# Kernel tuning notes

Measured on AMD Instinct MI355X. Metric: run time of the kernel, lower is better.

The kernel has to match this reference:

```python
import jax, jax.numpy as jnp
import numpy as np

B, N, S, T, H = 4, 6000, 48, 550, 128  # events, electrons, sensor grid, ticks, mlp hidden
INV_2PI = 1.0 / (2.0 * 3.14159)  # matches the source constant 3.14159
GAUSS_NORM = 0.3989422804


def setup_inputs() -> dict:
    key = jax.random.key(0)
    ks = jax.random.split(key, 9)
    simulator_input = jax.random.normal(ks[0], (B, N, 2), dtype=jnp.float32)
    z_positions = jax.random.uniform(ks[1], (B, N), dtype=jnp.float32) * (T - 1)
    mask = jnp.ones((B, N, 1), dtype=jnp.float32)
    # 48x48 sensor plane spanning [-5, 5] in x and y
    lin = jnp.linspace(-5.0, 5.0, S, dtype=jnp.float32)
    sensor_locations = jnp.stack(jnp.meshgrid(lin, lin, indexing='ij'), axis=-1)  # [S,S,2]
    # MLP params (2 -> H -> H -> 1)
    W1 = jax.random.normal(ks[2], (2, H), dtype=jnp.float32) * (1.0 / np.sqrt(2.0))
    b1 = jnp.zeros((H,), dtype=jnp.float32)
    W2 = jax.random.normal(ks[3], (H, H), dtype=jnp.float32) * (1.0 / np.sqrt(H))
    b2 = jnp.zeros((H,), dtype=jnp.float32)
    W3 = jax.random.normal(ks[4], (H, 1), dtype=jnp.float32) * (1.0 / np.sqrt(H))
    b3 = jnp.zeros((1,), dtype=jnp.float32)
    el_spread = jnp.ones((1,), dtype=jnp.float32)
    nn_bin_sigma = jnp.ones((1,), dtype=jnp.float32)
    return {
        'simulator_input': simulator_input, 'z_positions': z_positions, 'mask': mask,
        'sensor_locations': sensor_locations,
        'W1': W1, 'b1': b1, 'W2': W2, 'b2': b2, 'W3': W3, 'b3': b3,
        'el_spread': el_spread, 'nn_bin_sigma': nn_bin_sigma,
    }


def reference(simulator_input, z_positions, mask, sensor_locations,
              W1, b1, W2, b2, W3, b3, el_spread, nn_bin_sigma):
    # EL simulator MLP -> exp -> mask  ([B,N,1])
    h = jax.nn.relu(simulator_input @ W1 + b1)
    h = jax.nn.relu(h @ W2 + b2)
    resp = jnp.exp(h @ W3 + b3) * mask

    # Spatial gaussian splat onto sensor plane: [B,N,S,S]
    diff = simulator_input[:, :, None, None, :] - sensor_locations  # [B,N,S,S,2]
    r2 = jnp.sum(diff * diff, axis=-1)
    variance = el_spread ** 2  # (1,)
    spread = jnp.exp(-0.5 * (r2 / variance)) * (INV_2PI / variance)
    sr = spread * resp[..., None]  # [B,N,S,S]

    # Temporal gaussian over waveform ticks: [B,N,T]
    ticks = jnp.arange(T, dtype=simulator_input.dtype)  # linspace(0, T-1, T)
    bs = nn_bin_sigma ** 2  # (1,)
    ev = jnp.exp(-((ticks[None, None, :] - z_positions[:, :, None]) ** 2) / (2.0 * bs))
    ev = ev * (GAUSS_NORM / jnp.sqrt(bs))

    # Matmul reduce over electrons, then sum over batch: [S,S,T]
    return jnp.einsum('bnpq,bnt->pqt', sr, ev)
```

## Files before the change

### kernel.cpp

```cpp
#include <hip/hip_runtime.h>
#include <math.h>

#define BB 4
#define NN 6000
#define BN (BB*NN)
#define SS 48
#define PQ (SS*SS)
#define TT 550
#define HH 128

#define TPQ 128
#define TTILE 64
#define NTILES 9
#define KT 16
#define SPLITK 8
#define CAP 6144
#define MLP_E 64

__device__ __constant__ float kINV_2PI = 1.0f / (2.0f * 3.14159f);
__device__ __constant__ float kGAUSS_NORM = 0.3989422804f;
#define LOG2E 1.4426950408889634f

__device__ __forceinline__ float fexp2(float x) { return __builtin_amdgcn_exp2f(x); }

__global__ __launch_bounds__(256) void prep_kernel(
    const float* __restrict__ si, const float* __restrict__ zpos,
    const float* __restrict__ mask,
    const float* __restrict__ W1, const float* __restrict__ b1,
    const float* __restrict__ W2, const float* __restrict__ b2,
    const float* __restrict__ W3, const float* __restrict__ b3,
    const float* __restrict__ sensor, const float* __restrict__ el_spread,
    const float* __restrict__ nn_bin_sigma,
    int* __restrict__ counts,
    float* __restrict__ GxT, float* __restrict__ GyT, float* __restrict__ zT)
{
  __shared__ float sh1T[HH][MLP_E];
  __shared__ float sW1[2 * HH];
  __shared__ float sb1[HH], sb2[HH], sW3[HH];
  __shared__ float sex[MLP_E], sey[MLP_E], sresp[MLP_E], slin[SS];
  __shared__ int   sSlot[NTILES][MLP_E];
  int tid = threadIdx.x;
  if (tid < 2 * HH) sW1[tid] = W1[tid];
  if (tid < HH) { sb1[tid] = b1[tid]; sb2[tid] = b2[tid]; sW3[tid] = W3[tid]; }
  if (tid < SS) slin[tid] = sensor[tid * SS * 2];
  int e0 = blockIdx.x * MLP_E;
  int e = tid & 63;
  float x0 = si[2 * (e0 + e)], x1 = si[2 * (e0 + e) + 1];
  if (tid < MLP_E) { sex[tid] = x0; sey[tid] = x1; }
  __syncthreads();
  int jb = (tid >> 6) * 32;
  #pragma unroll
  for (int jj = 0; jj < 32; ++jj) {
    int j = jb + jj;
    sh1T[j][e] = fmaxf(x0 * sW1[j] + x1 * sW1[HH + j] + sb1[j], 0.0f);
  }
  __syncthreads();
  int c4 = (tid & 31) * 4;
  int eh = tid >> 5;
  float acc[8][4] = {};
  for (int i = 0; i < HH; ++i) {
    float4 w  = *(const float4*)&W2[i * HH + c4];
    float4 ha = *(const float4*)&sh1T[i][eh * 8];
    float4 hb = *(const float4*)&sh1T[i][eh * 8 + 4];
    float hv[8] = {ha.x, ha.y, ha.z, ha.w, hb.x, hb.y, hb.z, hb.w};
    #pragma unroll
    for (int ee = 0; ee < 8; ++ee) {
      acc[ee][0] += hv[ee] * w.x; acc[ee][1] += hv[ee] * w.y;
      acc[ee][2] += hv[ee] * w.z; acc[ee][3] += hv[ee] * w.w;
    }
  }
  float outp[8];
  #pragma unroll
  for (int ee = 0; ee < 8; ++ee) {
    float sacc = 0.0f;
    #pragma unroll
    for (int cc = 0; cc < 4; ++cc)
      sacc += fmaxf(acc[ee][cc] + sb2[c4 + cc], 0.0f) * sW3[c4 + cc];
    outp[ee] = sacc;
  }
  #pragma unroll
  for (int off = 1; off < 32; off <<= 1)
    #pragma unroll
    for (int ee = 0; ee < 8; ++ee)
      outp[ee] += __shfl_xor(outp[ee], off);
  if ((tid & 31) == 0) {
    float b3v = b3[0];
    #pragma unroll
    for (int ee = 0; ee < 8; ++ee) {
      int eidx = e0 + eh * 8 + ee;
      sresp[eh * 8 + ee] = fexp2((outp[ee] + b3v) * LOG2E) * mask[eidx];
    }
  }
  __syncthreads();
  if (tid < 64) {
    float sbv = nn_bin_sigma[0];
    float bs = sbv * sbv;
    float Wz = ceilf(sqrtf(128.0f * bs));
    float z = zpos[e0 + tid];
    int jlo = (int)floorf((z - Wz) * (1.0f / TTILE));
    int jhi = (int)floorf((z + Wz) * (1.0f / TTILE));
    jlo = jlo < 0 ? 0 : jlo;
    jhi = jhi > NTILES - 1 ? NTILES - 1 : jhi;
    int lane = tid;
    for (int j = 0; j < NTILES; ++j) {
      bool c = (j >= jlo) && (j <= jhi);
      unsigned long long m = __ballot(c);
      int s = -1;
      if (m != 0ull) {
        int leader = __ffsll(m) - 1;
        int base = 0;
        if (lane == leader) base = atomicAdd(&counts[j], __popcll(m));
        base = __shfl(base, leader);
        if (c) {
          int slot = base + __popcll(m & ((1ull << lane) - 1ull));
          if (slot < CAP) { s = slot; zT[j * CAP + slot] = z; }
        }
      }
      sSlot[j][lane] = s;
    }
  }
  __syncthreads();
  float es = el_spread[0];
  float var = es * es;
  float c = (0.5f / var) * LOG2E;
  float sbv = nn_bin_sigma[0];
  float bs = sbv * sbv;
  float amul = (kINV_2PI / var) * (kGAUSS_NORM / sqrtf(bs));
  for (int v = tid; v < MLP_E * SS; v += 256) {
    int ei = v / SS;
    int p = v - ei * SS;
    float lp = slin[p];
    float dx = sex[ei] - lp, dy = sey[ei] - lp;
    float gx = fexp2(-dx * dx * c) * sresp[ei] * amul;
    float gy = fexp2(-dy * dy * c);
    #pragma unroll
    for (int j = 0; j < NTILES; ++j) {
      int s = sSlot[j][ei];
      if (s >= 0) {
        GxT[(j * CAP + s) * SS + p] = gx;
        GyT[(j * CAP + s) * SS + p] = gy;
      }
    }
  }
}

__global__ __launch_bounds__(256) void gemm_kernel(
    const float* __restrict__ GxT, const float* __restrict__ GyT,
    const float* __restrict__ zT, const int* __restrict__ counts,
    const float* __restrict__ nn_bin_sigma, float* __restrict__ part)
{
  __shared__ __attribute__((aligned(16))) float Asm[KT][TPQ];
  __shared__ __attribute__((aligned(16))) float Esm[KT][TTILE];

  int tid = threadIdx.x;
  int pqBase = blockIdx.x * TPQ;
  int tileT = blockIdx.y;
  int tBase = tileT * TTILE;
  int bz = blockIdx.z;

  float s = nn_bin_sigma[0];
  float c2 = (0.5f * LOG2E) / (s * s);

  int count = counts[tileT];
  if (count > CAP) count = CAP;
  int chunks = (count + KT - 1) / KT;
  int cpsBase = chunks / SPLITK;
  int rem = chunks - cpsBase * SPLITK;
  int myC = cpsBase + (bz < rem ? 1 : 0);
  int chunk0 = bz * cpsBase + (bz < rem ? bz : rem);
  int k0 = chunk0 * KT;
  int kend = k0 + myC * KT;

  const float* __restrict__ Gxb = GxT + tileT * CAP * SS;
  const float* __restrict__ Gyb = GyT + tileT * CAP * SS;
  const float* __restrict__ zb  = zT + tileT * CAP;

  int aR = tid >> 5;
  int aC = (tid & 31) * 4;
  int eR = tid >> 4;
  int eC = (tid & 15) * 4;
  int tpq = (tid >> 4) * 8;
  int tt  = (tid & 15) * 4;

  int pqc = pqBase + aC;
  int p0 = pqc / SS,       q0 = pqc - p0 * SS;
  int p1 = (pqc+1) / SS,   q1 = (pqc+1) - p1 * SS;
  int p2 = (pqc+2) / SS,   q2 = (pqc+2) - p2 * SS;
  int p3 = (pqc+3) / SS,   q3 = (pqc+3) - p3 * SS;

  float acc[8][4] = {};

  for (int kc = k0; kc < kend; kc += KT) {
    #pragma unroll
    for (int pass = 0; pass < 2; ++pass) {
      int k = kc + aR + pass * 8;
      float4 av = make_float4(0.f, 0.f, 0.f, 0.f);
      if (k < count) {
        const float* gxr = Gxb + k * SS;
        const float* gyr = Gyb + k * SS;
        av.x = gxr[p0] * gyr[q0];
        av.y = gxr[p1] * gyr[q1];
        av.z = gxr[p2] * gyr[q2];
        av.w = gxr[p3] * gyr[q3];
      }
      *(float4*)&Asm[aR + pass * 8][aC] = av;
    }
    {
      int ek = kc + eR;
      float z = (ek < count) ? zb[ek] : -1.0e6f;
      float d0 = (float)(tBase + eC)     - z;
      float d1 = (float)(tBase + eC + 1) - z;
      float d2 = (float)(tBase + eC + 2) - z;
      float d3 = (float)(tBase + eC + 3) - z;
      *(float4*)&Esm[eR][eC] =
          make_float4(fexp2(-d0 * d0 * c2), fexp2(-d1 * d1 * c2),
                      fexp2(-d2 * d2 * c2), fexp2(-d3 * d3 * c2));
    }
    __syncthreads();
    #pragma unroll
    for (int k2 = 0; k2 < KT; ++k2) {
      float4 a0 = *(const float4*)&Asm[k2][tpq];
      float4 a1 = *(const float4*)&Asm[k2][tpq + 4];
      float4 e4 = *(const float4*)&Esm[k2][tt];
      float aa[8] = {a0.x, a0.y, a0.z, a0.w, a1.x, a1.y, a1.z, a1.w};
      float ee[4] = {e4.x, e4.y, e4.z, e4.w};
      #pragma unroll
      for (int i2 = 0; i2 < 8; ++i2)
        #pragma unroll
        for (int j2 = 0; j2 < 4; ++j2)
          acc[i2][j2] += aa[i2] * ee[j2];
    }
    __syncthreads();
  }

  float* pb = part + ((tileT * SPLITK + bz) * PQ) * TTILE;
  #pragma unroll
  for (int i = 0; i < 8; ++i) {
    int pq = pqBase + tpq + i;
    *(float4*)&pb[pq * TTILE + tt] =
        make_float4(acc[i][0], acc[i][1], acc[i][2], acc[i][3]);
  }
}

__global__ __launch_bounds__(256) void reduce_kernel(
    const float* __restrict__ part, float* __restrict__ out)
{
  int i = blockIdx.x * 256 + threadIdx.x;
  if (i >= PQ * TT) return;
  int pq = i / TT;
  int t = i - pq * TT;
  int tileT = t >> 6;
  int tl = t & 63;
  const float* p = part + ((tileT * SPLITK) * PQ + pq) * TTILE + tl;
  float sum = 0.0f;
  #pragma unroll
  for (int s2 = 0; s2 < SPLITK; ++s2)
    sum += p[s2 * (PQ * TTILE)];
  out[i] = sum;
}

extern "C" void kernel_launch(void* const* d_in, const int* in_sizes, int n_in,
                              void* d_out, int out_size, void* d_ws, size_t ws_size,
                              hipStream_t stream) {
  const float* si     = (const float*)d_in[0];
  const float* zpos   = (const float*)d_in[1];
  const float* mask   = (const float*)d_in[2];
  const float* sensor = (const float*)d_in[3];
  const float* W1     = (const float*)d_in[4];
  const float* b1     = (const float*)d_in[5];
  const float* W2     = (const float*)d_in[6];
  const float* b2     = (const float*)d_in[7];
  const float* W3     = (const float*)d_in[8];
  const float* b3     = (const float*)d_in[9];
  const float* el_spread    = (const float*)d_in[10];
  const float* nn_bin_sigma = (const float*)d_in[11];
  float* out = (float*)d_out;

  float* ws    = (float*)d_ws;
  float* part  = ws;
  float* GxT   = part + NTILES * SPLITK * PQ * TTILE;
  float* GyT   = GxT + NTILES * CAP * SS;
  float* zT    = GyT + NTILES * CAP * SS;
  int*   counts = (int*)(zT + NTILES * CAP);

  hipMemsetAsync(counts, 0, 16 * sizeof(int), stream);
  prep_kernel<<<BN / MLP_E, 256, 0, stream>>>(si, zpos, mask, W1, b1, W2, b2, W3, b3,
                                              sensor, el_spread, nn_bin_sigma,
                                              counts, GxT, GyT, zT);
  gemm_kernel<<<dim3(PQ / TPQ, NTILES, SPLITK), 256, 0, stream>>>(
      GxT, GyT, zT, counts, nn_bin_sigma, part);
  reduce_kernel<<<(PQ * TT + 255) / 256, 256, 0, stream>>>(part, out);
}
```

Baseline: 320.5 us.

## Use 96-wide pq tiles aligned to sensor rows with vectorized Gy loads

```diff
diff --git a/kernel.cpp b/kernel.cpp
--- a/kernel.cpp
+++ b/kernel.cpp
@@ -9,7 +9,7 @@
 #define TT 550
 #define HH 128
 
-#define TPQ 128
+#define TPQ 96
 #define TTILE 64
 #define NTILES 9
 #define KT 16
@@ -144,7 +144,7 @@
   }
 }
 
-__global__ __launch_bounds__(256) void gemm_kernel(
+__global__ __launch_bounds__(256, 8) void gemm_kernel(
     const float* __restrict__ GxT, const float* __restrict__ GyT,
     const float* __restrict__ zT, const int* __restrict__ counts,
     const float* __restrict__ nn_bin_sigma, float* __restrict__ part)
@@ -154,6 +154,7 @@
 
   int tid = threadIdx.x;
   int pqBase = blockIdx.x * TPQ;
+  int pBase = pqBase / SS;
   int tileT = blockIdx.y;
   int tBase = tileT * TTILE;
   int bz = blockIdx.z;
@@ -175,35 +176,39 @@
   const float* __restrict__ Gyb = GyT + tileT * CAP * SS;
   const float* __restrict__ zb  = zT + tileT * CAP;
 
-  int aR = tid >> 5;
-  int aC = (tid & 31) * 4;
+  int r0 = tid / 24,          c0 = (tid - r0 * 24) * 4;
+  int t2 = tid + 256;
+  int r1 = t2 / 24,           c1 = (t2 - r1 * 24) * 4;
+  int pl0 = (c0 >= SS) ? 1 : 0, ql0 = c0 - pl0 * SS;
+  int pl1 = (c1 >= SS) ? 1 : 0, ql1 = c1 - pl1 * SS;
+
   int eR = tid >> 4;
   int eC = (tid & 15) * 4;
-  int tpq = (tid >> 4) * 8;
+  int tpq = (tid >> 4) * 6;
   int tt  = (tid & 15) * 4;
 
-  int pqc = pqBase + aC;
-  int p0 = pqc / SS,       q0 = pqc - p0 * SS;
-  int p1 = (pqc+1) / SS,   q1 = (pqc+1) - p1 * SS;
-  int p2 = (pqc+2) / SS,   q2 = (pqc+2) - p2 * SS;
-  int p3 = (pqc+3) / SS,   q3 = (pqc+3) - p3 * SS;
-
-  float acc[8][4] = {};
+  float acc[6][4] = {};
 
   for (int kc = k0; kc < kend; kc += KT) {
-    #pragma unroll
-    for (int pass = 0; pass < 2; ++pass) {
-      int k = kc + aR + pass * 8;
+    {
+      int k = kc + r0;
       float4 av = make_float4(0.f, 0.f, 0.f, 0.f);
       if (k < count) {
-        const float* gxr = Gxb + k * SS;
-        const float* gyr = Gyb + k * SS;
-        av.x = gxr[p0] * gyr[q0];
-        av.y = gxr[p1] * gyr[q1];
-        av.z = gxr[p2] * gyr[q2];
-        av.w = gxr[p3] * gyr[q3];
-      }
-      *(float4*)&Asm[aR + pass * 8][aC] = av;
+        float4 gy = *(const float4*)&Gyb[k * SS + ql0];
+        float gxv = Gxb[k * SS + pBase + pl0];
+        av = make_float4(gxv * gy.x, gxv * gy.y, gxv * gy.z, gxv * gy.w);
+      }
+      *(float4*)&Asm[r0][c0] = av;
+    }
+    if (tid < 128) {
+      int k = kc + r1;
+      float4 av = make_float4(0.f, 0.f, 0.f, 0.f);
+      if (k < count) {
+        float4 gy = *(const float4*)&Gyb[k * SS + ql1];
+        float gxv = Gxb[k * SS + pBase + pl1];
+        av = make_float4(gxv * gy.x, gxv * gy.y, gxv * gy.z, gxv * gy.w);
+      }
+      *(float4*)&Asm[r1][c1] = av;
     }
     {
       int ek = kc + eR;
@@ -220,12 +225,12 @@
     #pragma unroll
     for (int k2 = 0; k2 < KT; ++k2) {
       float4 a0 = *(const float4*)&Asm[k2][tpq];
-      float4 a1 = *(const float4*)&Asm[k2][tpq + 4];
+      float2 a1 = *(const float2*)&Asm[k2][tpq + 4];
       float4 e4 = *(const float4*)&Esm[k2][tt];
-      float aa[8] = {a0.x, a0.y, a0.z, a0.w, a1.x, a1.y, a1.z, a1.w};
+      float aa[6] = {a0.x, a0.y, a0.z, a0.w, a1.x, a1.y};
       float ee[4] = {e4.x, e4.y, e4.z, e4.w};
       #pragma unroll
-      for (int i2 = 0; i2 < 8; ++i2)
+      for (int i2 = 0; i2 < 6; ++i2)
         #pragma unroll
         for (int j2 = 0; j2 < 4; ++j2)
           acc[i2][j2] += aa[i2] * ee[j2];
@@ -235,7 +240,7 @@
 
   float* pb = part + ((tileT * SPLITK + bz) * PQ) * TTILE;
   #pragma unroll
-  for (int i = 0; i < 8; ++i) {
+  for (int i = 0; i < 6; ++i) {
     int pq = pqBase + tpq + i;
     *(float4*)&pb[pq * TTILE + tt] =
         make_float4(acc[i][0], acc[i][1], acc[i][2], acc[i][3]);
```

Measured after the change: 292.0 us. -8.9%, faster.
